# Optimization experiments

Measured on AMD Instinct MI355X. Metric: run time of the kernel, lower is better.

## Reference

```python
import jax, jax.numpy as jnp
import numpy as np

EPS_BN = 1e-5
EPS_LN = 1e-5
EPS_L2 = 1e-12


def adder2d(x, w, stride):
    """AdderNet pseudo-conv: out = -sum |x_patch - w| (negative L1 distance).
    x: (N, Cin, H, W); w: (Cout, Cin, kh, kw); no padding, no bias.
    Loops only over the small fixed kernel footprint (<=12 positions) to avoid
    materializing the full im2col L1 tensor at once.
    """
    N, Cin, H, W = x.shape
    Cout, _, kh, kw = w.shape
    sh, sw = stride
    Ho = (H - kh) // sh + 1
    Wo = (W - kw) // sw + 1
    out = jnp.zeros((N, Ho, Wo, Cout), dtype=x.dtype)
    for i in range(kh):
        for j in range(kw):
            # strided slice of the input for this kernel tap: (N, Cin, Ho, Wo)
            xs = x[:, :, i:i + sh * Ho:sh, j:j + sw * Wo:sw]
            xs = jnp.transpose(xs, (0, 2, 3, 1))          # (N, Ho, Wo, Cin)
            wt = w[:, :, i, j]                            # (Cout, Cin)
            # |x - w| summed over Cin -> (N, Ho, Wo, Cout)
            out = out - jnp.abs(xs[:, :, :, None, :] - wt[None, None, None, :, :]).sum(-1)
    return jnp.transpose(out, (0, 3, 1, 2))               # (N, Cout, Ho, Wo)


def bn_relu(x, gamma, beta):
    # training-mode BatchNorm2d (batch statistics, biased var) + ReLU
    mean = x.mean(axis=(0, 2, 3), keepdims=True)
    var = x.var(axis=(0, 2, 3), keepdims=True)
    y = (x - mean) * jax.lax.rsqrt(var + EPS_BN)
    y = y * gamma[None, :, None, None] + beta[None, :, None, None]
    return jax.nn.relu(y)


def setup_inputs() -> dict:
    key = jax.random.key(0)
    ks = jax.random.split(key, 8)
    N = 16
    x = jax.random.normal(ks[0], (N, 1, 196, 3), dtype=jnp.float32)
    w1 = jax.random.normal(ks[1], (128, 1, 6, 1), dtype=jnp.float32) * 0.1
    w2 = jax.random.normal(ks[2], (256, 128, 6, 1), dtype=jnp.float32) * 0.05
    w3 = jax.random.normal(ks[3], (384, 256, 6, 2), dtype=jnp.float32) * 0.05
    g1, b1 = jnp.ones((128,), jnp.float32), jnp.zeros((128,), jnp.float32)
    g2, b2 = jnp.ones((256,), jnp.float32), jnp.zeros((256,), jnp.float32)
    g3, b3 = jnp.ones((384,), jnp.float32), jnp.zeros((384,), jnp.float32)
    Wfc = jax.random.normal(ks[4], (6, 16128), dtype=jnp.float32) * (1.0 / np.sqrt(16128))
    bfc = jax.random.normal(ks[5], (6,), dtype=jnp.float32) * 0.01
    return {"x": x, "w1": w1, "g1": g1, "b1": b1, "w2": w2, "g2": g2, "b2": b2,
            "w3": w3, "g3": g3, "b3": b3, "Wfc": Wfc, "bfc": bfc}


def reference(x, w1, g1, b1, w2, g2, b2, w3, g3, b3, Wfc, bfc):
    h = bn_relu(adder2d(x, w1, (2, 1)), g1, b1)   # (N,128,96,3)
    h = bn_relu(adder2d(h, w2, (2, 1)), g2, b2)   # (N,256,46,3)
    h = bn_relu(adder2d(h, w3, (2, 1)), g3, b3)   # (N,384,21,2)
    h = h.reshape(h.shape[0], -1)                  # (N,16128)
    h = h @ Wfc.T + bfc                            # (N,6)
    # nn.LayerNorm(x.size()) normalizes over ALL dims (batch included), weight=1 bias=0
    mu = h.mean()
    var = h.var()
    h = (h - mu) * jax.lax.rsqrt(var + EPS_LN)
    # F.normalize: per-row L2 normalization
    norm = jnp.sqrt((h * h).sum(axis=1, keepdims=True))
    return h / jnp.maximum(norm, EPS_L2)
```

## Files before the change

### kernel.cpp

```cpp
#include <hip/hip_runtime.h>
#include <math.h>

#define DEVINL __device__ __forceinline__

DEVINL float absadd(float a, float b) {
  float t;
  asm("v_add_f32 %0, |%1|, |%2|" : "=v"(t) : "v"(a), "v"(b));
  return t;
}

template<int NWAVES>
DEVINL void block_reduce_2d(double& a, double& b) {
  #pragma unroll
  for (int off = 32; off > 0; off >>= 1) {
    a += __shfl_down(a, off, 64);
    b += __shfl_down(b, off, 64);
  }
  __shared__ double sa[NWAVES], sb[NWAVES];
  const int tid = threadIdx.x;
  const int wid = tid >> 6;
  if ((tid & 63) == 0) { sa[wid] = a; sb[wid] = b; }
  __syncthreads();
  if (tid == 0) {
    double ta = 0.0, tb = 0.0;
    #pragma unroll
    for (int w = 0; w < NWAVES; ++w) { ta += sa[w]; tb += sb[w]; }
    a = ta; b = tb;
  }
}

__global__ __launch_bounds__(256) void k_conv1(
    const float* __restrict__ x, const float* __restrict__ w1,
    const float* __restrict__ g1, const float* __restrict__ b1,
    float* __restrict__ h1) {
  __shared__ float xlds[9408];
  const int co = blockIdx.x;
  const int tid = threadIdx.x;
  {
    float4* xd = (float4*)xlds;
    const float4* xs = (const float4*)x;
    #pragma unroll
    for (int k = 0; k < 10; ++k) {
      const int f = tid + k * 256;
      if (f < 2352) xd[f] = xs[f];
    }
  }
  float wv[6];
  #pragma unroll
  for (int i = 0; i < 6; ++i) wv[i] = w1[co * 6 + i];
  __syncthreads();

  float vals[18];
  double s = 0.0, sq = 0.0;
  #pragma unroll
  for (int k = 0; k < 18; ++k) {
    const int p = tid + k * 256;
    const int n = p / 288;
    const int r = p - n * 288;
    const int ho = r / 3;
    const int wo = r - ho * 3;
    const float* xb = xlds + n * 588 + (2 * ho) * 3 + wo;
    float e0 = xb[0]  - wv[0];
    float e1 = xb[3]  - wv[1];
    float e2 = xb[6]  - wv[2];
    float e3 = xb[9]  - wv[3];
    float e4 = xb[12] - wv[4];
    float e5 = xb[15] - wv[5];
    const float t0 = absadd(e0, e1);
    const float t1 = absadd(e2, e3);
    const float t2 = absadd(e4, e5);
    const float v = -((t0 + t1) + t2);
    vals[k] = v;
    s += (double)v;
    sq += (double)v * (double)v;
  }
  block_reduce_2d<4>(s, sq);
  __shared__ float ssc, ssh;
  if (tid == 0) {
    const double mean = s * (1.0 / 4608.0);
    const double var  = sq * (1.0 / 4608.0) - mean * mean;
    const float rstd = (float)rsqrt(var + 1e-5);
    const float sc = g1[co] * rstd;
    ssc = sc;
    ssh = b1[co] - (float)mean * sc;
  }
  __syncthreads();
  const float sc = ssc, sh = ssh;
  #pragma unroll
  for (int k = 0; k < 18; ++k) {
    const int p = tid + k * 256;
    const int n = p / 288;
    const int r = p - n * 288;
    const int ho = r / 3;
    const int wo = r - ho * 3;
    h1[((n * 128 + co) * 96 + ho) * 3 + wo] = fmaxf(0.f, fmaf(vals[k], sc, sh));
  }
}

__global__ __launch_bounds__(256) void k_conv2p(
    const float* __restrict__ h1, const float* __restrict__ w2,
    float* __restrict__ part2) {
  __shared__ float wlds[1024];
  __shared__ float2 xbuf4[4][616];
  const int bx = blockIdx.x;
  const int kc = bx & 7;
  const int rbx = bx >> 3;
  const int cg = rbx & 31;
  const int rbx2 = rbx >> 5;
  const int hoh = rbx2 & 1;
  const int nh = rbx2 >> 1;
  const int co0 = cg * 8, ci0 = kc * 16, n0 = nh * 8;
  const int tid = threadIdx.x;
  const int wvid = tid >> 6;
  const int lane = tid & 63;
  #pragma unroll
  for (int k = 0; k < 4; ++k) {
    const int f = wvid * 256 + lane + k * 64;
    const int cil = f >> 6, rem = f & 63, c = rem >> 3, kk = rem & 7;
    wlds[f] = (kk < 6) ? w2[(co0 + c) * 768 + (ci0 + cil) * 6 + kk] : 0.f;
  }
  const int n = lane >> 3, co = lane & 7;

  int s_lds[10], s_g[10];
  const bool v10 = lane < 24;
  #pragma unroll
  for (int k = 0; k < 10; ++k) {
    const int f = lane + k * 64;
    const int nn = f / 75, j = f - nn * 75;
    s_lds[k] = nn * 77 + j;
    s_g[k]   = (n0 + nn) * 18432 + 69 * hoh + j;
  }
  const float2* h1v = (const float2*)h1;
  const int cibase = ci0 + wvid * 4;

  float acc[69];
  #pragma unroll
  for (int i = 0; i < 69; ++i) acc[i] = 0.f;

  float2 r[10];
  #pragma unroll
  for (int k = 0; k < 9; ++k) r[k] = h1v[s_g[k] + cibase * 144];
  if (v10) r[9] = h1v[s_g[9] + cibase * 144];

  const float2* xrow2 = xbuf4[wvid] + n * 77;
  const float4* wl4 = (const float4*)wlds;

  #pragma unroll 1
  for (int cil = 0; cil < 4; ++cil) {
    #pragma unroll
    for (int k = 0; k < 9; ++k) xbuf4[wvid][s_lds[k]] = r[k];
    if (v10) xbuf4[wvid][s_lds[9]] = r[9];
    if (cil + 1 < 4) {
      #pragma unroll
      for (int k = 0; k < 9; ++k) r[k] = h1v[s_g[k] + (cibase + cil + 1) * 144];
      if (v10) r[9] = h1v[s_g[9] + (cibase + cil + 1) * 144];
    }
    const int cl = wvid * 4 + cil;
    const float4 wa = wl4[(cl * 8 + co) * 2];
    const float4 wb = wl4[(cl * 8 + co) * 2 + 1];
    const float wv[6] = {wa.x, wa.y, wa.z, wa.w, wb.x, wb.y};
    float xf[18];
    #pragma unroll
    for (int t = 0; t < 9; ++t) {
      const float2 q = xrow2[t];
      xf[2 * t] = q.x; xf[2 * t + 1] = q.y;
    }
    #pragma unroll
    for (int h = 0; h < 23; ++h) {
      if (h > 0) {
        #pragma unroll
        for (int t = 0; t < 12; ++t) xf[t] = xf[t + 6];
        #pragma unroll
        for (int t = 0; t < 3; ++t) {
          const float2 q = xrow2[3 * h + 6 + t];
          xf[12 + 2 * t] = q.x; xf[13 + 2 * t] = q.y;
        }
      }
      #pragma unroll
      for (int wo = 0; wo < 3; ++wo) {
        float e0 = xf[0  + wo] - wv[0];
        float e1 = xf[3  + wo] - wv[1];
        float e2 = xf[6  + wo] - wv[2];
        float e3 = xf[9  + wo] - wv[3];
        float e4 = xf[12 + wo] - wv[4];
        float e5 = xf[15 + wo] - wv[5];
        const float t0 = absadd(e0, e1);
        const float t1 = absadd(e2, e3);
        const float t2 = absadd(e4, e5);
        acc[h * 3 + wo] += (t0 + t1) + t2;
      }
    }
  }
  __syncthreads();
  float* accb = (float*)xbuf4;
  #pragma unroll
  for (int chunk = 0; chunk < 3; ++chunk) {
    if (wvid > 0) {
      #pragma unroll
      for (int i = 0; i < 23; ++i)
        accb[((wvid - 1) * 64 + lane) * 24 + i] = acc[chunk * 23 + i];
    }
    __syncthreads();
    if (wvid == 0) {
      #pragma unroll
      for (int w = 0; w < 3; ++w)
        #pragma unroll
        for (int i = 0; i < 23; ++i)
          acc[chunk * 23 + i] += accb[(w * 64 + lane) * 24 + i];
    }
    __syncthreads();
  }
  if (wvid == 0) {
    float* dst = part2 + (size_t)(kc * 256 + co0 + co) * 2208 + (n0 + n) * 138 + 69 * hoh;
    #pragma unroll
    for (int i = 0; i < 69; ++i) dst[i] = acc[i];
  }
}

__global__ __launch_bounds__(384) void k_combine2(
    const float* __restrict__ part2, const float* __restrict__ g2,
    const float* __restrict__ b2, float* __restrict__ h2) {
  const int co = blockIdx.x;
  const int tid = threadIdx.x;
  const bool active = tid < 368;
  float v[6];
  double s = 0.0, sq = 0.0;
  #pragma unroll
  for (int k = 0; k < 6; ++k) {
    float sum = 0.f;
    if (active) {
      const int p = tid + k * 368;
      #pragma unroll
      for (int kc = 0; kc < 8; ++kc)
        sum += part2[(size_t)(kc * 256 + co) * 2208 + p];
    }
    const float val = -sum;
    v[k] = val;
    if (active) { s += (double)val; sq += (double)val * (double)val; }
  }
  block_reduce_2d<6>(s, sq);
  __shared__ float ssc, ssh;
  if (tid == 0) {
    const double mean = s * (1.0 / 2208.0);
    const double var  = sq * (1.0 / 2208.0) - mean * mean;
    const float rstd = (float)rsqrt(var + 1e-5);
    const float sc = g2[co] * rstd;
    ssc = sc;
    ssh = b2[co] - (float)mean * sc;
  }
  __syncthreads();
  if (active) {
    const float sc = ssc, sh = ssh;
    #pragma unroll
    for (int k = 0; k < 6; ++k) {
      const int p = tid + k * 368;
      const int n = p / 138, rem = p - n * 138;
      h2[n * 35328 + co * 138 + rem] = fmaxf(0.f, fmaf(v[k], sc, sh));
    }
  }
}

__global__ __launch_bounds__(256) void k_conv3p(
    const float* __restrict__ h2, const float* __restrict__ w3,
    float* __restrict__ part3) {
  __shared__ float wlds[1536];
  __shared__ float2 xbuf4[4][560];
  const int bx = blockIdx.x;
  const int kc = bx & 15;
  const int rbx = bx >> 4;
  const int cg = rbx % 48;
  const int nh = rbx / 48;
  const int co0 = cg * 8, ci0 = kc * 16, n0 = nh * 8;
  const int tid = threadIdx.x;
  const int wvid = tid >> 6;
  const int lane = tid & 63;
  #pragma unroll
  for (int k = 0; k < 6; ++k) {
    const int f = wvid * 384 + lane + k * 64;
    const int cil = f / 96, rem = f - cil * 96, c = rem / 12, kk = rem - c * 12;
    wlds[f] = w3[(co0 + c) * 3072 + (ci0 + cil) * 12 + kk];
  }
  const int n = lane >> 3, co = lane & 7;

  int s_lds[9], s_g[9];
  const bool v9 = lane < 40;
  #pragma unroll
  for (int k = 0; k < 9; ++k) {
    const int f = lane + k * 64;
    const int nn = f / 69, j = f - nn * 69;
    s_lds[k] = nn * 70 + j;
    s_g[k]   = (n0 + nn) * 17664 + j;
  }
  const float2* h2v = (const float2*)h2;
  const int cibase = ci0 + wvid * 4;

  float acc[42];
  #pragma unroll
  for (int i = 0; i < 42; ++i) acc[i] = 0.f;

  float2 r[9];
  #pragma unroll
  for (int k = 0; k < 8; ++k) r[k] = h2v[s_g[k] + cibase * 69];
  if (v9) r[8] = h2v[s_g[8] + cibase * 69];

  const float2* xrow2 = xbuf4[wvid] + n * 70;
  const float4* wl4 = (const float4*)wlds;

  #pragma unroll 1
  for (int cil = 0; cil < 4; ++cil) {
    #pragma unroll
    for (int k = 0; k < 8; ++k) xbuf4[wvid][s_lds[k]] = r[k];
    if (v9) xbuf4[wvid][s_lds[8]] = r[8];
    if (cil + 1 < 4) {
      #pragma unroll
      for (int k = 0; k < 8; ++k) r[k] = h2v[s_g[k] + (cibase + cil + 1) * 69];
      if (v9) r[8] = h2v[s_g[8] + (cibase + cil + 1) * 69];
    }
    const int cl = wvid * 4 + cil;
    const float4 w0 = wl4[(cl * 8 + co) * 3];
    const float4 w1 = wl4[(cl * 8 + co) * 3 + 1];
    const float4 w2q = wl4[(cl * 8 + co) * 3 + 2];
    const float wv[12] = {w0.x, w0.y, w0.z, w0.w, w1.x, w1.y,
                          w1.z, w1.w, w2q.x, w2q.y, w2q.z, w2q.w};
    float xf[30];
    #pragma unroll
    for (int t = 0; t < 15; ++t) {
      const float2 q = xrow2[t];
      xf[2 * t + 0] = q.x; xf[2 * t + 1] = q.y;
    }
    #pragma unroll
    for (int hot = 0; hot < 7; ++hot) {
      #pragma unroll
      for (int h = 0; h < 3; ++h)
        #pragma unroll
        for (int wo = 0; wo < 2; ++wo) {
          float e0  = xf[(2 * h + 0) * 3 + wo]     - wv[0];
          float e1  = xf[(2 * h + 0) * 3 + wo + 1] - wv[1];
          float e2  = xf[(2 * h + 1) * 3 + wo]     - wv[2];
          float e3  = xf[(2 * h + 1) * 3 + wo + 1] - wv[3];
          float e4  = xf[(2 * h + 2) * 3 + wo]     - wv[4];
          float e5  = xf[(2 * h + 2) * 3 + wo + 1] - wv[5];
          float e6  = xf[(2 * h + 3) * 3 + wo]     - wv[6];
          float e7  = xf[(2 * h + 3) * 3 + wo + 1] - wv[7];
          float e8  = xf[(2 * h + 4) * 3 + wo]     - wv[8];
          float e9  = xf[(2 * h + 4) * 3 + wo + 1] - wv[9];
          float e10 = xf[(2 * h + 5) * 3 + wo]     - wv[10];
          float e11 = xf[(2 * h + 5) * 3 + wo + 1] - wv[11];
          const float t0 = absadd(e0, e1);
          const float t1 = absadd(e2, e3);
          const float t2 = absadd(e4, e5);
          const float t3 = absadd(e6, e7);
          const float t4 = absadd(e8, e9);
          const float t5 = absadd(e10, e11);
          acc[(3 * hot + h) * 2 + wo] += ((t0 + t1) + (t2 + t3)) + (t4 + t5);
        }
      if (hot < 6) {
        #pragma unroll
        for (int t = 0; t < 12; ++t) xf[t] = xf[t + 18];
        #pragma unroll
        for (int t = 0; t < 9; ++t) {
          const float2 q = xrow2[9 * hot + 15 + t];
          xf[12 + 2 * t] = q.x; xf[13 + 2 * t] = q.y;
        }
      }
    }
  }
  __syncthreads();
  float* accb = (float*)xbuf4;
  #pragma unroll
  for (int chunk = 0; chunk < 2; ++chunk) {
    if (wvid > 0) {
      #pragma unroll
      for (int i = 0; i < 21; ++i)
        accb[((wvid - 1) * 64 + lane) * 22 + i] = acc[chunk * 21 + i];
    }
    __syncthreads();
    if (wvid == 0) {
      #pragma unroll
      for (int w = 0; w < 3; ++w)
        #pragma unroll
        for (int i = 0; i < 21; ++i)
          acc[chunk * 21 + i] += accb[(w * 64 + lane) * 22 + i];
    }
    __syncthreads();
  }
  if (wvid == 0) {
    float2* dst = (float2*)(part3 + (size_t)(kc * 384 + co0 + co) * 672 + (n0 + n) * 42);
    #pragma unroll
    for (int k = 0; k < 21; ++k) dst[k] = make_float2(acc[2 * k], acc[2 * k + 1]);
  }
}

__global__ __launch_bounds__(384) void k_combine3(
    const float* __restrict__ part3, const float* __restrict__ g3,
    const float* __restrict__ b3, float* __restrict__ h3) {
  const int co = blockIdx.x;
  const int tid = threadIdx.x;
  const bool active = tid < 336;
  float v[2];
  double s = 0.0, sq = 0.0;
  #pragma unroll
  for (int k = 0; k < 2; ++k) {
    float sum = 0.f;
    if (active) {
      const int p = tid + k * 336;
      #pragma unroll
      for (int kc = 0; kc < 16; ++kc)
        sum += part3[(size_t)(kc * 384 + co) * 672 + p];
    }
    const float val = -sum;
    v[k] = val;
    if (active) { s += (double)val; sq += (double)val * (double)val; }
  }
  block_reduce_2d<6>(s, sq);
  __shared__ float ssc, ssh;
  if (tid == 0) {
    const double mean = s * (1.0 / 672.0);
    const double var  = sq * (1.0 / 672.0) - mean * mean;
    const float rstd = (float)rsqrt(var + 1e-5);
    const float sc = g3[co] * rstd;
    ssc = sc;
    ssh = b3[co] - (float)mean * sc;
  }
  __syncthreads();
  if (active) {
    const float sc = ssc, sh = ssh;
    #pragma unroll
    for (int k = 0; k < 2; ++k) {
      const int p = tid + k * 336;
      const int n = p / 42, rem = p - n * 42;
      h3[n * 16128 + co * 42 + rem] = fmaxf(0.f, fmaf(v[k], sc, sh));
    }
  }
}

__global__ __launch_bounds__(256) void k_fcp(
    const float* __restrict__ h3, const float* __restrict__ Wfc,
    float* __restrict__ hfcp) {
  const int bx = blockIdx.x;
  const int pair = bx >> 2, q = bx & 3;
  const int n = pair / 6, o = pair - n * 6;
  const float4* xr = (const float4*)(h3 + n * 16128) + q * 1008;
  const float4* wr = (const float4*)(Wfc + o * 16128) + q * 1008;
  float sacc = 0.f;
  for (int k = threadIdx.x; k < 1008; k += 256) {
    const float4 xv = xr[k];
    const float4 wv = wr[k];
    sacc += xv.x * wv.x + xv.y * wv.y + xv.z * wv.z + xv.w * wv.w;
  }
  double d = (double)sacc, dummy = 0.0;
  block_reduce_2d<4>(d, dummy);
  if (threadIdx.x == 0) hfcp[bx] = (float)d;
}

__global__ __launch_bounds__(128) void k_final(
    const float* __restrict__ hfcp, const float* __restrict__ bfc,
    float* __restrict__ out) {
  __shared__ float ys[96];
  __shared__ float params[2];
  const int tid = threadIdx.x;
  float v = 0.f;
  if (tid < 96) {
    v = hfcp[tid * 4 + 0] + hfcp[tid * 4 + 1] + hfcp[tid * 4 + 2] + hfcp[tid * 4 + 3]
        + bfc[tid % 6];
    ys[tid] = v;
  }
  __syncthreads();
  if (tid == 0) {
    double s = 0.0, sq = 0.0;
    for (int i = 0; i < 96; ++i) { const double t = (double)ys[i]; s += t; sq += t * t; }
    const double mu = s / 96.0;
    const double var = sq / 96.0 - mu * mu;
    params[0] = (float)mu;
    params[1] = (float)rsqrt(var + 1e-5);
  }
  __syncthreads();
  const float y = (v - params[0]) * params[1];
  __syncthreads();
  if (tid < 96) ys[tid] = y;
  __syncthreads();
  if (tid < 96) {
    const int n = tid / 6;
    float ss = 0.f;
    #pragma unroll
    for (int k = 0; k < 6; ++k) { const float t = ys[n * 6 + k]; ss += t * t; }
    const float norm = sqrtf(ss);
    out[tid] = y / fmaxf(norm, 1e-12f);
  }
}

extern "C" void kernel_launch(void* const* d_in, const int* in_sizes, int n_in,
                              void* d_out, int out_size, void* d_ws, size_t ws_size,
                              hipStream_t stream) {
  const float* x   = (const float*)d_in[0];
  const float* w1  = (const float*)d_in[1];
  const float* g1  = (const float*)d_in[2];
  const float* b1  = (const float*)d_in[3];
  const float* w2  = (const float*)d_in[4];
  const float* g2  = (const float*)d_in[5];
  const float* b2  = (const float*)d_in[6];
  const float* w3  = (const float*)d_in[7];
  const float* g3  = (const float*)d_in[8];
  const float* b3  = (const float*)d_in[9];
  const float* Wfc = (const float*)d_in[10];
  const float* bfc = (const float*)d_in[11];

  float* ws   = (float*)d_ws;
  float* h1   = ws;
  float* h2   = h1 + 589824;
  float* h3   = h2 + 565248;
  float* hfcp = h3 + 258048;
  float* part = hfcp + 384;
  float* out  = (float*)d_out;

  k_conv1   <<<128, 256, 0, stream>>>(x, w1, g1, b1, h1);
  k_conv2p  <<<1024, 256, 0, stream>>>(h1, w2, part);
  k_combine2<<<256, 384, 0, stream>>>(part, g2, b2, h2);
  k_conv3p  <<<1536, 256, 0, stream>>>(h2, w3, part);
  k_combine3<<<384, 384, 0, stream>>>(part, g3, b3, h3);
  k_fcp     <<<384, 256, 0, stream>>>(h3, Wfc, hfcp);
  k_final   <<<1, 128, 0, stream>>>(hfcp, bfc, out);
}
```

Measured before the change: 106.1 us.

## Compute two output channels per thread in conv3 to reuse input registers

Each thread in the layer-3 adder conv now handles two output channels instead of one. Each block covers 16 channels, which halves the grid to 768 blocks and doubles the weight tile in LDS. The input sliding window is restructured to shift one output row at a time, so each loaded input value serves both channels and per-channel LDS reads are reduced. The cost is 84 accumulators per thread, which raises register pressure and may lower occupancy, plus fewer blocks to spread across CUs.

```diff
diff --git a/kernel.cpp b/kernel.cpp
--- a/kernel.cpp
+++ b/kernel.cpp
@@ -263,24 +263,24 @@
 __global__ __launch_bounds__(256) void k_conv3p(
     const float* __restrict__ h2, const float* __restrict__ w3,
     float* __restrict__ part3) {
-  __shared__ float wlds[1536];
+  __shared__ float wlds[3072];
   __shared__ float2 xbuf4[4][560];
   const int bx = blockIdx.x;
   const int kc = bx & 15;
   const int rbx = bx >> 4;
-  const int cg = rbx % 48;
-  const int nh = rbx / 48;
-  const int co0 = cg * 8, ci0 = kc * 16, n0 = nh * 8;
+  const int cg = rbx % 24;
+  const int nh = rbx / 24;
+  const int co0 = cg * 16, ci0 = kc * 16, n0 = nh * 8;
   const int tid = threadIdx.x;
   const int wvid = tid >> 6;
   const int lane = tid & 63;
   #pragma unroll
-  for (int k = 0; k < 6; ++k) {
-    const int f = wvid * 384 + lane + k * 64;
-    const int cil = f / 96, rem = f - cil * 96, c = rem / 12, kk = rem - c * 12;
+  for (int k = 0; k < 12; ++k) {
+    const int f = wvid * 768 + lane + k * 64;
+    const int cil = f / 192, rem = f - cil * 192, c = rem / 12, kk = rem - c * 12;
     wlds[f] = w3[(co0 + c) * 3072 + (ci0 + cil) * 12 + kk];
   }
-  const int n = lane >> 3, co = lane & 7;
+  const int n = lane >> 3, cp = lane & 7;
 
   int s_lds[9], s_g[9];
   const bool v9 = lane < 40;
@@ -294,9 +294,11 @@
   const float2* h2v = (const float2*)h2;
   const int cibase = ci0 + wvid * 4;
 
-  float acc[42];
-  #pragma unroll
-  for (int i = 0; i < 42; ++i) acc[i] = 0.f;
+  float acc[2][42];
+  #pragma unroll
+  for (int c2 = 0; c2 < 2; ++c2)
+    #pragma unroll
+    for (int i = 0; i < 42; ++i) acc[c2][i] = 0.f;
 
   float2 r[9];
   #pragma unroll
@@ -317,50 +319,76 @@
       if (v9) r[8] = h2v[s_g[8] + (cibase + cil + 1) * 69];
     }
     const int cl = wvid * 4 + cil;
-    const float4 w0 = wl4[(cl * 8 + co) * 3];
-    const float4 w1 = wl4[(cl * 8 + co) * 3 + 1];
-    const float4 w2q = wl4[(cl * 8 + co) * 3 + 2];
-    const float wv[12] = {w0.x, w0.y, w0.z, w0.w, w1.x, w1.y,
-                          w1.z, w1.w, w2q.x, w2q.y, w2q.z, w2q.w};
-    float xf[30];
-    #pragma unroll
-    for (int t = 0; t < 15; ++t) {
+    const float4 a0 = wl4[(cl * 16 + 2 * cp) * 3];
+    const float4 a1 = wl4[(cl * 16 + 2 * cp) * 3 + 1];
+    const float4 a2 = wl4[(cl * 16 + 2 * cp) * 3 + 2];
+    const float4 b0 = wl4[(cl * 16 + 2 * cp + 1) * 3];
+    const float4 b1 = wl4[(cl * 16 + 2 * cp + 1) * 3 + 1];
+    const float4 b2q = wl4[(cl * 16 + 2 * cp + 1) * 3 + 2];
+    const float wva[12] = {a0.x, a0.y, a0.z, a0.w, a1.x, a1.y,
+                           a1.z, a1.w, a2.x, a2.y, a2.z, a2.w};
+    const float wvb[12] = {b0.x, b0.y, b0.z, b0.w, b1.x, b1.y,
+                           b1.z, b1.w, b2q.x, b2q.y, b2q.z, b2q.w};
+    float xf[18];
+    #pragma unroll
+    for (int t = 0; t < 9; ++t) {
       const float2 q = xrow2[t];
-      xf[2 * t + 0] = q.x; xf[2 * t + 1] = q.y;
-    }
-    #pragma unroll
-    for (int hot = 0; hot < 7; ++hot) {
-      #pragma unroll
-      for (int h = 0; h < 3; ++h)
-        #pragma unroll
-        for (int wo = 0; wo < 2; ++wo) {
-          float e0  = xf[(2 * h + 0) * 3 + wo]     - wv[0];
-          float e1  = xf[(2 * h + 0) * 3 + wo + 1] - wv[1];
-          float e2  = xf[(2 * h + 1) * 3 + wo]     - wv[2];
-          float e3  = xf[(2 * h + 1) * 3 + wo + 1] - wv[3];
-          float e4  = xf[(2 * h + 2) * 3 + wo]     - wv[4];
-          float e5  = xf[(2 * h + 2) * 3 + wo + 1] - wv[5];
-          float e6  = xf[(2 * h + 3) * 3 + wo]     - wv[6];
-          float e7  = xf[(2 * h + 3) * 3 + wo + 1] - wv[7];
-          float e8  = xf[(2 * h + 4) * 3 + wo]     - wv[8];
-          float e9  = xf[(2 * h + 4) * 3 + wo + 1] - wv[9];
-          float e10 = xf[(2 * h + 5) * 3 + wo]     - wv[10];
-          float e11 = xf[(2 * h + 5) * 3 + wo + 1] - wv[11];
+      xf[2 * t] = q.x; xf[2 * t + 1] = q.y;
+    }
+    #pragma unroll
+    for (int ho = 0; ho < 21; ++ho) {
+      if (ho > 0) {
+        #pragma unroll
+        for (int t = 0; t < 12; ++t) xf[t] = xf[t + 6];
+        #pragma unroll
+        for (int t = 0; t < 3; ++t) {
+          const float2 q = xrow2[3 * ho + 6 + t];
+          xf[12 + 2 * t] = q.x; xf[13 + 2 * t] = q.y;
+        }
+      }
+      #pragma unroll
+      for (int wo = 0; wo < 2; ++wo) {
+        {
+          float e0  = xf[0  + wo] - wva[0];
+          float e1  = xf[1  + wo] - wva[1];
+          float e2  = xf[3  + wo] - wva[2];
+          float e3  = xf[4  + wo] - wva[3];
+          float e4  = xf[6  + wo] - wva[4];
+          float e5  = xf[7  + wo] - wva[5];
+          float e6  = xf[9  + wo] - wva[6];
+          float e7  = xf[10 + wo] - wva[7];
+          float e8  = xf[12 + wo] - wva[8];
+          float e9  = xf[13 + wo] - wva[9];
+          float e10 = xf[15 + wo] - wva[10];
+          float e11 = xf[16 + wo] - wva[11];
           const float t0 = absadd(e0, e1);
           const float t1 = absadd(e2, e3);
           const float t2 = absadd(e4, e5);
           const float t3 = absadd(e6, e7);
           const float t4 = absadd(e8, e9);
           const float t5 = absadd(e10, e11);
-          acc[(3 * hot + h) * 2 + wo] += ((t0 + t1) + (t2 + t3)) + (t4 + t5);
+          acc[0][ho * 2 + wo] += ((t0 + t1) + (t2 + t3)) + (t4 + t5);
         }
-      if (hot < 6) {
-        #pragma unroll
-        for (int t = 0; t < 12; ++t) xf[t] = xf[t + 18];
-        #pragma unroll
-        for (int t = 0; t < 9; ++t) {
-          const float2 q = xrow2[9 * hot + 15 + t];
-          xf[12 + 2 * t] = q.x; xf[13 + 2 * t] = q.y;
+        {
+          float e0  = xf[0  + wo] - wvb[0];
+          float e1  = xf[1  + wo] - wvb[1];
+          float e2  = xf[3  + wo] - wvb[2];
+          float e3  = xf[4  + wo] - wvb[3];
+          float e4  = xf[6  + wo] - wvb[4];
+          float e5  = xf[7  + wo] - wvb[5];
+          float e6  = xf[9  + wo] - wvb[6];
+          float e7  = xf[10 + wo] - wvb[7];
+          float e8  = xf[12 + wo] - wvb[8];
+          float e9  = xf[13 + wo] - wvb[9];
+          float e10 = xf[15 + wo] - wvb[10];
+          float e11 = xf[16 + wo] - wvb[11];
+          const float t0 = absadd(e0, e1);
+          const float t1 = absadd(e2, e3);
+          const float t2 = absadd(e4, e5);
+          const float t3 = absadd(e6, e7);
+          const float t4 = absadd(e8, e9);
+          const float t5 = absadd(e10, e11);
+          acc[1][ho * 2 + wo] += ((t0 + t1) + (t2 + t3)) + (t4 + t5);
         }
       }
     }
@@ -368,26 +396,34 @@
   __syncthreads();
   float* accb = (float*)xbuf4;
   #pragma unroll
-  for (int chunk = 0; chunk < 2; ++chunk) {
-    if (wvid > 0) {
-      #pragma unroll
-      for (int i = 0; i < 21; ++i)
-        accb[((wvid - 1) * 64 + lane) * 22 + i] = acc[chunk * 21 + i];
-    }
-    __syncthreads();
-    if (wvid == 0) {
-      #pragma unroll
-      for (int w = 0; w < 3; ++w)
+  for (int c2 = 0; c2 < 2; ++c2) {
+    #pragma unroll
+    for (int half = 0; half < 2; ++half) {
+      if (wvid > 0) {
         #pragma unroll
         for (int i = 0; i < 21; ++i)
-          acc[chunk * 21 + i] += accb[(w * 64 + lane) * 22 + i];
-    }
-    __syncthreads();
+          accb[((wvid - 1) * 64 + lane) * 22 + i] = acc[c2][half * 21 + i];
+      }
+      __syncthreads();
+      if (wvid == 0) {
+        #pragma unroll
+        for (int w = 0; w < 3; ++w)
+          #pragma unroll
+          for (int i = 0; i < 21; ++i)
+            acc[c2][half * 21 + i] += accb[(w * 64 + lane) * 22 + i];
+      }
+      __syncthreads();
+    }
   }
   if (wvid == 0) {
-    float2* dst = (float2*)(part3 + (size_t)(kc * 384 + co0 + co) * 672 + (n0 + n) * 42);
-    #pragma unroll
-    for (int k = 0; k < 21; ++k) dst[k] = make_float2(acc[2 * k], acc[2 * k + 1]);
+    #pragma unroll
+    for (int c2 = 0; c2 < 2; ++c2) {
+      float2* dst = (float2*)(part3 +
+          (size_t)(kc * 384 + co0 + 2 * cp + c2) * 672 + (n0 + n) * 42);
+      #pragma unroll
+      for (int k = 0; k < 21; ++k)
+        dst[k] = make_float2(acc[c2][2 * k], acc[c2][2 * k + 1]);
+    }
   }
 }
 
@@ -516,7 +552,7 @@
   k_conv1   <<<128, 256, 0, stream>>>(x, w1, g1, b1, h1);
   k_conv2p  <<<1024, 256, 0, stream>>>(h1, w2, part);
   k_combine2<<<256, 384, 0, stream>>>(part, g2, b2, h2);
-  k_conv3p  <<<1536, 256, 0, stream>>>(h2, w3, part);
+  k_conv3p  <<<768, 256, 0, stream>>>(h2, w3, part);
   k_combine3<<<384, 384, 0, stream>>>(part, g3, b3, h3);
   k_fcp     <<<384, 256, 0, stream>>>(h3, Wfc, hfcp);
   k_final   <<<1, 128, 0, stream>>>(hfcp, bfc, out);
```

New measurement: 110.6 us. 4.3% more time.
